# Performance work log

Measured on AMD Instinct MI355X. Metric: run time of the kernel, lower is better.

The kernel has to match this reference:

```python
import jax, jax.numpy as jnp
import numpy as np

N = 100000      # nodes (single node type)
R = 4           # relations
E = 800000      # edges per relation (avg in-degree ~32)
D_IN, D_H, D_OUT = 256, 64, 16


def setup_inputs() -> dict:
    key = jax.random.key(0)
    ks = jax.random.split(key, 9)
    x = jax.random.normal(ks[0], (N, D_IN), dtype=jnp.float32)
    src = jax.random.randint(ks[1], (R, E), 0, N, dtype=jnp.int32)
    dst = jax.random.randint(ks[2], (R, E), 0, N, dtype=jnp.int32)
    s_in = 1.0 / np.sqrt(D_IN)
    s_h = 1.0 / np.sqrt(D_H)
    W1 = jax.random.normal(ks[3], (R, D_IN, D_H), dtype=jnp.float32) * s_in
    L1w = jax.random.normal(ks[4], (D_IN, D_H), dtype=jnp.float32) * s_in
    L1b = jnp.zeros((D_H,), dtype=jnp.float32)
    W2 = jax.random.normal(ks[5], (R, D_H, D_OUT), dtype=jnp.float32) * s_h
    L2w = jax.random.normal(ks[6], (D_H, D_OUT), dtype=jnp.float32) * s_h
    L2b = jnp.zeros((D_OUT,), dtype=jnp.float32)
    return {"x": x, "src": src, "dst": dst, "W1": W1, "L1w": L1w,
            "L1b": L1b, "W2": W2, "L2w": L2w, "L2b": L2b}


def _rel_graph_conv(h, src, dst, W):
    """Per-relation GEMM + gather + scatter-add + right-normalize, summed over relations.
    h: [N, d_in]; src/dst: [R, E]; W: [R, d_in, d_out] -> [N, d_out]
    """
    hw = jnp.einsum('nd,rdh->rnh', h, W)  # transform first (d_out small), then gather

    def agg(hr, s, d):
        deg = jax.ops.segment_sum(jnp.ones((E,), hr.dtype), d, num_segments=N)
        msg = jax.ops.segment_sum(hr[s], d, num_segments=N)  # [N, d_out]
        return msg / jnp.maximum(deg, 1.0)[:, None]          # norm='right'

    return jnp.sum(jax.vmap(agg)(hw, src, dst), axis=0)


def reference(x, src, dst, W1, L1w, L1b, W2, L2w, L2b):
    # Layer 1: relation conv + self-loop linear + ReLU (dropout = eval/identity)
    h = _rel_graph_conv(x, src, dst, W1) + x @ L1w + L1b
    h = jax.nn.relu(h)
    # Layer 2: no activation
    out = _rel_graph_conv(h, src, dst, W2) + h @ L2w + L2b
    return out
```

## Files before the change

### kernel.cpp

```cpp
#include <hip/hip_runtime.h>


constexpr int NN = 100000, RR = 4, EE = 800000;
constexpr int RE = RR * EE;
constexpr int NBKT = (NN + 63) / 64;
constexpr int BCAP = 3072;
constexpr int NG1 = (NN + 63) / 64;
constexpr int CHUNK = 8192;
constexpr int NB = (RE + CHUNK - 1) / CHUNK;
constexpr int EPT = CHUNK / 512;

typedef short bf16x8 __attribute__((ext_vector_type(8)));
typedef float f32x4 __attribute__((ext_vector_type(4)));

__device__ inline unsigned short f2bf(float f) {
  unsigned u = __float_as_uint(f);
  u += 0x7FFF + ((u >> 16) & 1);
  return (unsigned short)(u >> 16);
}
__device__ inline float bf2f(unsigned short s) {
  return __uint_as_float(((unsigned)s) << 16);
}

__global__ __launch_bounds__(256) void prep_w_kernel(const float* __restrict__ W1,
                                                     const float* __restrict__ L1w,
                                                     const float* __restrict__ W2,
                                                     const float* __restrict__ L2w,
                                                     unsigned short* __restrict__ BT1,
                                                     unsigned short* __restrict__ BT2) {
  int idx = blockIdx.x * 256 + threadIdx.x;
  if (idx < 320 * 256) {
    int n = idx >> 8, k = idx & 255;
    float v = (n < 256) ? W1[((size_t)((n >> 6) * 256 + k)) * 64 + (n & 63)]
                        : L1w[(size_t)k * 64 + (n - 256)];
    BT1[idx] = f2bf(v);
  } else {
    int j = idx - 320 * 256;
    if (j < 80 * 64) {
      int n = j >> 6, k = j & 63;
      float v = (n < 64) ? W2[((size_t)((n >> 4) * 64 + k)) * 16 + (n & 15)]
                         : L2w[(size_t)k * 16 + (n - 64)];
      BT2[j] = f2bf(v);
    }
  }
}

__global__ __launch_bounds__(512) void fused1_kernel(const float* __restrict__ x,
                                                     const unsigned short* __restrict__ BT1,
                                                     const float* __restrict__ L1b,
                                                     const int* __restrict__ src,
                                                     const int* __restrict__ dst,
                                                     int* __restrict__ gcur,
                                                     int* __restrict__ binned,
                                                     unsigned short* __restrict__ hwcat,
                                                     unsigned short* __restrict__ h) {
  __shared__ char lds[49152];
  const int bid = blockIdx.x;
  const int t = threadIdx.x;
  const bool is_bin = (bid % 5 == 0) && (bid / 5 < NB);

  if (is_bin) {
    int* hist = (int*)lds;
    int* base = hist + NBKT;
    for (int k = t; k < NBKT; k += 512) hist[k] = 0;
    __syncthreads();
    const int e0 = (bid / 5) * CHUNK + t;
    int dl[EPT], sl[EPT];
#pragma unroll
    for (int i = 0; i < EPT; ++i) {
      int fl = e0 + i * 512;
      dl[i] = -1;
      if (fl < RE) {
        dl[i] = dst[fl];
        sl[i] = src[fl];
        atomicAdd(&hist[dl[i] >> 6], 1);
      }
    }
    __syncthreads();
    for (int k = t; k < NBKT; k += 512) {
      int hv = hist[k];
      base[k] = hv ? atomicAdd(&gcur[k], hv) : 0;
      hist[k] = 0;
    }
    __syncthreads();
#pragma unroll
    for (int i = 0; i < EPT; ++i) {
      if (dl[i] < 0) continue;
      int fl = e0 + i * 512;
      int r = fl / EE;
      int b = dl[i] >> 6;
      int off = atomicAdd(&hist[b], 1);
      int p = base[b] + off;
      if (p < BCAP) binned[(size_t)b * BCAP + p] = (sl[i] << 2) | r | ((dl[i] & 63) << 19);
    }
    return;
  }

  int nbins = (bid + 4) / 5;
  if (nbins > NB) nbins = NB;
  const int m0 = (bid - nbins) * 64;
  char* Al = lds;
  char* Bl = lds + 64 * 64 * 2;
  const int wid = t >> 6, lane = t & 63;
  const int wm = wid >> 2, wn = wid & 3;
  const int l15 = lane & 15, g = lane >> 4;

  f32x4 acc[2][5];
#pragma unroll
  for (int i = 0; i < 2; ++i)
#pragma unroll
    for (int j = 0; j < 5; ++j) acc[i][j] = (f32x4){0.f, 0.f, 0.f, 0.f};

  for (int kc = 0; kc < 4; ++kc) {
    if (kc) __syncthreads();
#pragma unroll
    for (int it = 0; it < 2; ++it) {
      int fl = t + 512 * it;
      int row = fl >> 4, kq = (fl & 15) * 4;
      int rg = m0 + row;
      float4 v = (rg < NN) ? *(const float4*)(x + (size_t)rg * 256 + kc * 64 + kq)
                           : make_float4(0.f, 0.f, 0.f, 0.f);
      ushort4 pck = {f2bf(v.x), f2bf(v.y), f2bf(v.z), f2bf(v.w)};
      int wb = ((row * 64 + kq) * 2) ^ ((row & 7) << 4);
      *(ushort4*)(Al + wb) = pck;
    }
#pragma unroll
    for (int it = 0; it < 5; ++it) {
      int fl = t + 512 * it;
      int n = fl >> 3, i8 = (fl & 7) * 8;
      uint4 u = *(const uint4*)(BT1 + (size_t)n * 256 + kc * 64 + i8);
      int wb = ((n * 64 + i8) * 2) ^ ((n & 7) << 4);
      *(uint4*)(Bl + wb) = u;
    }
    __syncthreads();
#pragma unroll
    for (int ks = 0; ks < 2; ++ks) {
      bf16x8 af[2], bfr[5];
#pragma unroll
      for (int mi = 0; mi < 2; ++mi) {
        int row = wm * 32 + mi * 16 + l15;
        int byte = ((row * 64 + ks * 32 + g * 8) * 2) ^ ((row & 7) << 4);
        af[mi] = *(const bf16x8*)(Al + byte);
      }
#pragma unroll
      for (int ni = 0; ni < 5; ++ni) {
        int n = wn * 80 + ni * 16 + l15;
        int byte = ((n * 64 + ks * 32 + g * 8) * 2) ^ ((n & 7) << 4);
        bfr[ni] = *(const bf16x8*)(Bl + byte);
      }
#pragma unroll
      for (int mi = 0; mi < 2; ++mi)
#pragma unroll
        for (int ni = 0; ni < 5; ++ni)
          acc[mi][ni] = __builtin_amdgcn_mfma_f32_16x16x32_bf16(af[mi], bfr[ni], acc[mi][ni], 0, 0, 0);
    }
  }
#pragma unroll
  for (int mi = 0; mi < 2; ++mi) {
    int rbase = m0 + wm * 32 + mi * 16 + 4 * g;
#pragma unroll
    for (int ni = 0; ni < 5; ++ni) {
      int n0 = wn * 80 + ni * 16;
      int n = n0 + l15;
#pragma unroll
      for (int e = 0; e < 4; ++e) {
        int row = rbase + e;
        if (row >= NN) continue;
        float v = acc[mi][ni][e];
        if (n0 < 256) hwcat[(size_t)row * 256 + n] = f2bf(v);
        else h[(size_t)row * 64 + (n - 256)] = f2bf(v + L1b[n - 256]);
      }
    }
  }
}

__global__ __launch_bounds__(256) void pull1_kernel(const unsigned short* __restrict__ h,
                                                    const unsigned short* __restrict__ hwcat,
                                                    const int* __restrict__ binned,
                                                    const int* __restrict__ gcur,
                                                    const unsigned short* __restrict__ BT2,
                                                    const float* __restrict__ L2b,
                                                    unsigned short* __restrict__ hw2,
                                                    float* __restrict__ out) {
  __shared__ int csr[BCAP];
  __shared__ int cnt[256];
  __shared__ int off[256];
  __shared__ float winv[256];
  __shared__ int tot[64];
  __shared__ char Al[64 * 64 * 2];
  const int t = threadIdx.x, bkt = blockIdx.x;
  const int wid = t >> 6, lane = t & 63;
  const int l15 = lane & 15, g = lane >> 4;

  int count = gcur[bkt];
  if (count > BCAP) count = BCAP;
  const int* edges = binned + (size_t)bkt * BCAP;

  cnt[t] = 0;
  __syncthreads();
  for (int i = t; i < count; i += 256) {
    int w = edges[i];
    atomicAdd(&cnt[((w >> 19) & 63) * 4 + (w & 3)], 1);
  }
  __syncthreads();
  off[t] = cnt[t];
  __syncthreads();
  for (int s = 1; s < 256; s <<= 1) {
    int v = (t >= s) ? off[t - s] : 0;
    __syncthreads();
    off[t] += v;
    __syncthreads();
  }
  int excl = off[t] - cnt[t];
  winv[t] = 1.0f / (float)(cnt[t] > 1 ? cnt[t] : 1);
  __syncthreads();
  off[t] = excl;
  cnt[t] = excl;
  __syncthreads();
  if (t < 64) tot[t] = ((t == 63) ? count : off[(t + 1) * 4]) - off[t * 4];
  __syncthreads();
  for (int i = t; i < count; i += 256) {
    int w = edges[i];
    int k = ((w >> 19) & 63) * 4 + (w & 3);
    int p = atomicAdd(&cnt[k], 1);
    csr[p] = w & 0x7FFFF;
  }
  __syncthreads();

  const int slot = lane >> 3, cpart = lane & 7;
  for (int ii = 0; ii < 16; ++ii) {
    int nloc = wid * 16 + ii;
    int beg = off[nloc * 4];
    int total = tot[nloc];
    float acc[8] = {0.f, 0.f, 0.f, 0.f, 0.f, 0.f, 0.f, 0.f};
    for (int p0 = 0; p0 < total; p0 += 8) {
      int j = p0 + slot;
      bool pr = j < total;
      int key = pr ? csr[beg + j] : 0;
      float wv = pr ? winv[nloc * 4 + (key & 3)] : 0.f;
      uint4 u = *(const uint4*)(hwcat + (size_t)key * 64 + cpart * 8);
#pragma unroll
      for (int q = 0; q < 4; ++q) {
        unsigned uu = (&u.x)[q];
        acc[q * 2]     = fmaf(wv, bf2f((unsigned short)(uu & 0xffffu)), acc[q * 2]);
        acc[q * 2 + 1] = fmaf(wv, bf2f((unsigned short)(uu >> 16)), acc[q * 2 + 1]);
      }
    }
#pragma unroll
    for (int m = 8; m <= 32; m <<= 1)
#pragma unroll
      for (int q = 0; q < 8; ++q) acc[q] += __shfl_xor(acc[q], m);
    if (slot == 0) {
      int gn = bkt * 64 + nloc;
      unsigned pk[4];
      uint4 hu = make_uint4(0, 0, 0, 0);
      if (gn < NN) hu = *(const uint4*)(h + (size_t)gn * 64 + cpart * 8);
#pragma unroll
      for (int q = 0; q < 4; ++q) {
        unsigned a = (&hu.x)[q];
        float v0 = acc[q * 2]     + bf2f((unsigned short)(a & 0xffffu));
        float v1 = acc[q * 2 + 1] + bf2f((unsigned short)(a >> 16));
        pk[q] = (unsigned)f2bf(fmaxf(v0, 0.f)) | ((unsigned)f2bf(fmaxf(v1, 0.f)) << 16);
      }
      int wb = ((nloc * 64 + cpart * 8) * 2) ^ ((nloc & 7) << 4);
      *(uint4*)(Al + wb) = make_uint4(pk[0], pk[1], pk[2], pk[3]);
    }
  }
  __syncthreads();

  char* Bl = (char*)csr;
#pragma unroll
  for (int it = 0; it < 3; ++it) {
    int fl = t + 256 * it;
    if (fl < 640) {
      int n = fl >> 3, i8 = (fl & 7) * 8;
      uint4 u = *(const uint4*)(BT2 + (size_t)n * 64 + i8);
      int wb = ((n * 64 + i8) * 2) ^ ((n & 7) << 4);
      *(uint4*)(Bl + wb) = u;
    }
  }
  __syncthreads();

  f32x4 acc2[5];
#pragma unroll
  for (int j = 0; j < 5; ++j) acc2[j] = (f32x4){0.f, 0.f, 0.f, 0.f};
#pragma unroll
  for (int ks = 0; ks < 2; ++ks) {
    int ra = wid * 16 + l15;
    int byte = ((ra * 64 + ks * 32 + g * 8) * 2) ^ ((ra & 7) << 4);
    bf16x8 af = *(const bf16x8*)(Al + byte);
#pragma unroll
    for (int ni = 0; ni < 5; ++ni) {
      int n = ni * 16 + l15;
      int nb = ((n * 64 + ks * 32 + g * 8) * 2) ^ ((n & 7) << 4);
      bf16x8 bfr = *(const bf16x8*)(Bl + nb);
      acc2[ni] = __builtin_amdgcn_mfma_f32_16x16x32_bf16(af, bfr, acc2[ni], 0, 0, 0);
    }
  }
  int rb = wid * 16 + 4 * g;
#pragma unroll
  for (int ni = 0; ni < 5; ++ni) {
    int n0 = ni * 16;
    int n = n0 + l15;
#pragma unroll
    for (int e = 0; e < 4; ++e) {
      int gno = bkt * 64 + rb + e;
      if (gno >= NN) continue;
      float vv = acc2[ni][e];
      if (n0 < 64) hw2[(size_t)gno * 64 + n] = f2bf(vv);
      else out[(size_t)gno * 16 + (n - 64)] = vv + L2b[n - 64];
    }
  }
}

__global__ __launch_bounds__(256) void pull2_kernel(const unsigned short* __restrict__ hw2,
                                                    const int* __restrict__ binned,
                                                    const int* __restrict__ gcur,
                                                    float* __restrict__ out) {
  __shared__ int csr[BCAP];
  __shared__ int cnt[256];
  __shared__ int off[256];
  __shared__ float winv[256];
  __shared__ int tot[64];
  __shared__ float ot[64][16];
  const int t = threadIdx.x, bkt = blockIdx.x;
  const int wid = t >> 6, lane = t & 63;

  int count = gcur[bkt];
  if (count > BCAP) count = BCAP;
  const int* edges = binned + (size_t)bkt * BCAP;

  cnt[t] = 0;
  __syncthreads();
  for (int i = t; i < count; i += 256) {
    int w = edges[i];
    atomicAdd(&cnt[((w >> 19) & 63) * 4 + (w & 3)], 1);
  }
  __syncthreads();
  off[t] = cnt[t];
  __syncthreads();
  for (int s = 1; s < 256; s <<= 1) {
    int v = (t >= s) ? off[t - s] : 0;
    __syncthreads();
    off[t] += v;
    __syncthreads();
  }
  int excl = off[t] - cnt[t];
  winv[t] = 1.0f / (float)(cnt[t] > 1 ? cnt[t] : 1);
  __syncthreads();
  off[t] = excl;
  cnt[t] = excl;
  __syncthreads();
  if (t < 64) tot[t] = ((t == 63) ? count : off[(t + 1) * 4]) - off[t * 4];
  __syncthreads();
  for (int i = t; i < count; i += 256) {
    int w = edges[i];
    int k = ((w >> 19) & 63) * 4 + (w & 3);
    int p = atomicAdd(&cnt[k], 1);
    csr[p] = w & 0x7FFFF;
  }
  __syncthreads();

  const int slot = lane >> 2, cpart = lane & 3;
  for (int ii = 0; ii < 16; ++ii) {
    int nloc = wid * 16 + ii;
    int beg = off[nloc * 4];
    int total = tot[nloc];
    float acc[4] = {0.f, 0.f, 0.f, 0.f};
    for (int p0 = 0; p0 < total; p0 += 16) {
      int j = p0 + slot;
      bool pr = j < total;
      int key = pr ? csr[beg + j] : 0;
      float wv = pr ? winv[nloc * 4 + (key & 3)] : 0.f;
      uint2 u = *(const uint2*)(hw2 + (size_t)key * 16 + cpart * 4);
      acc[0] = fmaf(wv, bf2f((unsigned short)(u.x & 0xffffu)), acc[0]);
      acc[1] = fmaf(wv, bf2f((unsigned short)(u.x >> 16)), acc[1]);
      acc[2] = fmaf(wv, bf2f((unsigned short)(u.y & 0xffffu)), acc[2]);
      acc[3] = fmaf(wv, bf2f((unsigned short)(u.y >> 16)), acc[3]);
    }
#pragma unroll
    for (int m = 4; m <= 32; m <<= 1)
#pragma unroll
      for (int q = 0; q < 4; ++q) acc[q] += __shfl_xor(acc[q], m);
    if (slot == 0)
      *(float4*)&ot[nloc][cpart * 4] = make_float4(acc[0], acc[1], acc[2], acc[3]);
  }
  __syncthreads();

  int row = t >> 2, q = t & 3;
  int gn = bkt * 64 + row;
  if (gn < NN) {
    float4 o = *(float4*)(out + (size_t)gn * 16 + q * 4);
    float4 a = *(float4*)&ot[row][q * 4];
    o.x += a.x; o.y += a.y; o.z += a.z; o.w += a.w;
    *(float4*)(out + (size_t)gn * 16 + q * 4) = o;
  }
}

extern "C" void kernel_launch(void* const* d_in, const int* in_sizes, int n_in,
                              void* d_out, int out_size, void* d_ws, size_t ws_size,
                              hipStream_t stream) {
  const float* x   = (const float*)d_in[0];
  const int*   src = (const int*)d_in[1];
  const int*   dst = (const int*)d_in[2];
  const float* W1  = (const float*)d_in[3];
  const float* L1w = (const float*)d_in[4];
  const float* L1b = (const float*)d_in[5];
  const float* W2  = (const float*)d_in[6];
  const float* L2w = (const float*)d_in[7];
  const float* L2b = (const float*)d_in[8];
  float* out = (float*)d_out;

  char* p = (char*)d_ws;
  int* binned = (int*)p;                      p += (size_t)NBKT * BCAP * 4;
  int* gcur   = (int*)p;                      p += 8192;
  unsigned short* hwcat = (unsigned short*)p; p += (size_t)NN * 256 * 2;
  unsigned short* h = (unsigned short*)p;     p += (size_t)NN * 64 * 2;
  unsigned short* hw2 = (unsigned short*)p;   p += (size_t)NN * 64 * 2;
  unsigned short* BT1 = (unsigned short*)p;   p += 320 * 256 * 2;
  unsigned short* BT2 = (unsigned short*)p;   p += 80 * 64 * 2;
  if ((size_t)(p - (char*)d_ws) > ws_size) return;

  hipMemsetAsync(gcur, 0, NBKT * 4, stream);
  prep_w_kernel<<<(320 * 256 + 80 * 64 + 255) / 256, 256, 0, stream>>>(W1, L1w, W2, L2w, BT1, BT2);
  fused1_kernel<<<NG1 + NB, 512, 0, stream>>>(x, BT1, L1b, src, dst, gcur, binned, hwcat, h);
  pull1_kernel<<<NBKT, 256, 0, stream>>>(h, hwcat, binned, gcur, BT2, L2b, hw2, out);
  pull2_kernel<<<NBKT, 256, 0, stream>>>(hw2, binned, gcur, out);
}
```

Measured before the change: 229.7 us.

## Sort binned edges locally in LDS before coalesced global scatter

The binning blocks now prefix-scan the per-bucket histogram, sort each chunk's edges by bucket in LDS, and then write them to the global bins in bucket-contiguous order, so the global stores are more coalesced than the earlier random scatter. The chunk size is halved and the interleave ratio of binning to GEMM blocks changes from 1:4 to 1:2 so the LDS staging fits. This adds a block scan and extra LDS traffic and launches more binning blocks, each with more global atomics per edge than before.

```diff
diff --git a/kernel.cpp b/kernel.cpp
--- a/kernel.cpp
+++ b/kernel.cpp
@@ -6,7 +6,7 @@
 constexpr int NBKT = (NN + 63) / 64;
 constexpr int BCAP = 3072;
 constexpr int NG1 = (NN + 63) / 64;
-constexpr int CHUNK = 8192;
+constexpr int CHUNK = 4096;
 constexpr int NB = (RE + CHUNK - 1) / CHUNK;
 constexpr int EPT = CHUNK / 512;
 
@@ -57,14 +57,20 @@
   __shared__ char lds[49152];
   const int bid = blockIdx.x;
   const int t = threadIdx.x;
-  const bool is_bin = (bid % 5 == 0) && (bid / 5 < NB);
+  const bool is_bin = (bid % 3 == 0) && (bid / 3 < NB);
 
   if (is_bin) {
-    int* hist = (int*)lds;
-    int* base = hist + NBKT;
+    int* hist   = (int*)lds;
+    int* delta  = (int*)(lds + 6400);
+    int* sorted = (int*)(lds + 12800);
+    short* bkt16 = (short*)(lds + 29184);
+    int* wsum   = (int*)(lds + 37376);
+    int* ptots  = (int*)(lds + 37440);
+    const int wid = t >> 6, lane = t & 63;
+
     for (int k = t; k < NBKT; k += 512) hist[k] = 0;
     __syncthreads();
-    const int e0 = (bid / 5) * CHUNK + t;
+    const int e0 = (bid / 3) * CHUNK + t;
     int dl[EPT], sl[EPT];
 #pragma unroll
     for (int i = 0; i < EPT; ++i) {
@@ -77,10 +83,40 @@
       }
     }
     __syncthreads();
-    for (int k = t; k < NBKT; k += 512) {
-      int hv = hist[k];
-      base[k] = hv ? atomicAdd(&gcur[k], hv) : 0;
-      hist[k] = 0;
+    int cnt4[4];
+    int s = 0;
+#pragma unroll
+    for (int j = 0; j < 4; ++j) {
+      int b = t * 4 + j;
+      cnt4[j] = (b < NBKT) ? hist[b] : 0;
+      s += cnt4[j];
+    }
+    int xs = s;
+#pragma unroll
+    for (int d = 1; d < 64; d <<= 1) {
+      int y = __shfl_up(xs, d);
+      if (lane >= d) xs += y;
+    }
+    if (lane == 63) wsum[wid] = xs;
+    __syncthreads();
+    int add = 0;
+#pragma unroll
+    for (int w = 0; w < 8; ++w)
+      if (w < wid) add += wsum[w];
+    if (t == 511) *ptots = xs + add;
+    int lb = xs + add - s;
+#pragma unroll
+    for (int j = 0; j < 4; ++j) {
+      int b = t * 4 + j;
+      if (b < NBKT) {
+        int c = cnt4[j];
+        if (c > 0) {
+          int gb = atomicAdd(&gcur[b], c);
+          delta[b] = gb - lb;
+          hist[b] = lb;
+        }
+        lb += c;
+      }
     }
     __syncthreads();
 #pragma unroll
@@ -89,18 +125,28 @@
       int fl = e0 + i * 512;
       int r = fl / EE;
       int b = dl[i] >> 6;
-      int off = atomicAdd(&hist[b], 1);
-      int p = base[b] + off;
-      if (p < BCAP) binned[(size_t)b * BCAP + p] = (sl[i] << 2) | r | ((dl[i] & 63) << 19);
+      int p = atomicAdd(&hist[b], 1);
+      sorted[p] = (sl[i] << 2) | r | ((dl[i] & 63) << 19);
+      bkt16[p] = (short)b;
+    }
+    __syncthreads();
+    int ptot = *ptots;
+#pragma unroll
+    for (int i = 0; i < EPT; ++i) {
+      int p = t + i * 512;
+      if (p >= ptot) break;
+      int b = bkt16[p];
+      int inb = delta[b] + p;
+      if (inb < BCAP) binned[(size_t)b * BCAP + inb] = sorted[p];
     }
     return;
   }
 
-  int nbins = (bid + 4) / 5;
+  int nbins = (bid + 2) / 3;
   if (nbins > NB) nbins = NB;
   const int m0 = (bid - nbins) * 64;
   char* Al = lds;
-  char* Bl = lds + 64 * 64 * 2;
+  char* Bl = lds + 8192;
   const int wid = t >> 6, lane = t & 63;
   const int wm = wid >> 2, wn = wid & 3;
   const int l15 = lane & 15, g = lane >> 4;
```

New measurement: 241.1 us. +5.0%, slower.

## Replace single-pass edge binning with two-pass coarse-then-fine radix scatter

Applied to the files above, without the earlier changes.

Edge binning now runs as two radix passes. The fused kernel sorts each chunk locally by 49 coarse buckets (2048 destinations each) and writes contiguous runs into a coarse buffer. A new pass2 kernel then splits each coarse bucket into 32 fine 64-node bins. The aim is to replace the scattered per-edge global writes and the 1563-entry histogram with coalesced block-sorted writes and fewer global atomics. In exchange it adds an extra kernel launch and a full read/write of the edge list through the coarse buffer.

```diff
diff --git a/kernel.cpp b/kernel.cpp
--- a/kernel.cpp
+++ b/kernel.cpp
@@ -5,8 +5,11 @@
 constexpr int RE = RR * EE;
 constexpr int NBKT = (NN + 63) / 64;
 constexpr int BCAP = 3072;
+constexpr int NCOARSE = 49;
+constexpr int CCAP = 69632;
+constexpr int NCH = 17;
 constexpr int NG1 = (NN + 63) / 64;
-constexpr int CHUNK = 8192;
+constexpr int CHUNK = 4096;
 constexpr int NB = (RE + CHUNK - 1) / CHUNK;
 constexpr int EPT = CHUNK / 512;
 
@@ -50,21 +53,26 @@
                                                      const float* __restrict__ L1b,
                                                      const int* __restrict__ src,
                                                      const int* __restrict__ dst,
-                                                     int* __restrict__ gcur,
-                                                     int* __restrict__ binned,
+                                                     int* __restrict__ gcoarse,
+                                                     int* __restrict__ cbuf,
                                                      unsigned short* __restrict__ hwcat,
                                                      unsigned short* __restrict__ h) {
   __shared__ char lds[49152];
   const int bid = blockIdx.x;
   const int t = threadIdx.x;
-  const bool is_bin = (bid % 5 == 0) && (bid / 5 < NB);
+  const bool is_bin = (bid % 3 == 0) && (bid / 3 < NB);
 
   if (is_bin) {
     int* hist = (int*)lds;
-    int* base = hist + NBKT;
-    for (int k = t; k < NBKT; k += 512) hist[k] = 0;
-    __syncthreads();
-    const int e0 = (bid / 5) * CHUNK + t;
+    int* cur = hist + 64;
+    int* delta = cur + 64;
+    int* sorted = delta + 64;
+    unsigned char* cb = (unsigned char*)(sorted + 4096);
+    const int fid = bid / 3;
+
+    if (t < 64) hist[t] = 0;
+    __syncthreads();
+    const int e0 = fid * CHUNK + t;
     int dl[EPT], sl[EPT];
 #pragma unroll
     for (int i = 0; i < EPT; ++i) {
@@ -73,14 +81,24 @@
       if (fl < RE) {
         dl[i] = dst[fl];
         sl[i] = src[fl];
-        atomicAdd(&hist[dl[i] >> 6], 1);
-      }
-    }
-    __syncthreads();
-    for (int k = t; k < NBKT; k += 512) {
-      int hv = hist[k];
-      base[k] = hv ? atomicAdd(&gcur[k], hv) : 0;
-      hist[k] = 0;
+        atomicAdd(&hist[dl[i] >> 11], 1);
+      }
+    }
+    __syncthreads();
+    if (t < 64) {
+      int c = (t < NCOARSE) ? hist[t] : 0;
+      int xs = c;
+#pragma unroll
+      for (int d = 1; d < 64; d <<= 1) {
+        int y = __shfl_up(xs, d);
+        if (t >= d) xs += y;
+      }
+      int excl = xs - c;
+      if (t < NCOARSE) {
+        cur[t] = excl;
+        int gb = (c > 0) ? atomicAdd(&gcoarse[t], c) : 0;
+        delta[t] = gb - excl;
+      }
     }
     __syncthreads();
 #pragma unroll
@@ -88,19 +106,31 @@
       if (dl[i] < 0) continue;
       int fl = e0 + i * 512;
       int r = fl / EE;
-      int b = dl[i] >> 6;
-      int off = atomicAdd(&hist[b], 1);
-      int p = base[b] + off;
-      if (p < BCAP) binned[(size_t)b * BCAP + p] = (sl[i] << 2) | r | ((dl[i] & 63) << 19);
+      int cg = dl[i] >> 11;
+      int p = atomicAdd(&cur[cg], 1);
+      sorted[p] = (sl[i] << 2) | r | ((dl[i] & 2047) << 19);
+      cb[p] = (unsigned char)cg;
+    }
+    __syncthreads();
+    int ptot = RE - fid * CHUNK;
+    if (ptot > CHUNK) ptot = CHUNK;
+#pragma unroll
+    for (int i = 0; i < EPT; ++i) {
+      int p = t + i * 512;
+      if (p < ptot) {
+        int cg = cb[p];
+        int inb = delta[cg] + p;
+        if (inb < CCAP) cbuf[(size_t)cg * CCAP + inb] = sorted[p];
+      }
     }
     return;
   }
 
-  int nbins = (bid + 4) / 5;
+  int nbins = (bid + 2) / 3;
   if (nbins > NB) nbins = NB;
   const int m0 = (bid - nbins) * 64;
   char* Al = lds;
-  char* Bl = lds + 64 * 64 * 2;
+  char* Bl = lds + 8192;
   const int wid = t >> 6, lane = t & 63;
   const int wm = wid >> 2, wn = wid & 3;
   const int l15 = lane & 15, g = lane >> 4;
@@ -170,6 +200,71 @@
         if (n0 < 256) hwcat[(size_t)row * 256 + n] = f2bf(v);
         else h[(size_t)row * 64 + (n - 256)] = f2bf(v + L1b[n - 256]);
       }
+    }
+  }
+}
+
+__global__ __launch_bounds__(512) void pass2_kernel(const int* __restrict__ cbuf,
+                                                    const int* __restrict__ gcoarse,
+                                                    int* __restrict__ gcur,
+                                                    int* __restrict__ binned) {
+  __shared__ int hist32[32], cur32[32], delta32[32];
+  __shared__ int sorted[4096];
+  __shared__ unsigned char cb[4096];
+  const int t = threadIdx.x;
+  const int g = blockIdx.x / NCH, ch = blockIdx.x % NCH;
+  int count = gcoarse[g];
+  if (count > CCAP) count = CCAP;
+  const int base = ch * 4096;
+  int nhere = count - base;
+  if (nhere <= 0) return;
+  if (nhere > 4096) nhere = 4096;
+
+  if (t < 32) hist32[t] = 0;
+  __syncthreads();
+  int wl[8], fl8[8];
+#pragma unroll
+  for (int i = 0; i < 8; ++i) {
+    int j = t + i * 512;
+    fl8[i] = -1;
+    if (j < nhere) {
+      int w = cbuf[(size_t)g * CCAP + base + j];
+      wl[i] = w;
+      fl8[i] = (w >> 25) & 31;
+      atomicAdd(&hist32[fl8[i]], 1);
+    }
+  }
+  __syncthreads();
+  if (t < 32) {
+    int c = hist32[t];
+    int xs = c;
+#pragma unroll
+    for (int d = 1; d < 32; d <<= 1) {
+      int y = __shfl_up(xs, d);
+      if (t >= d) xs += y;
+    }
+    int excl = xs - c;
+    cur32[t] = excl;
+    int gb = (c > 0) ? atomicAdd(&gcur[g * 32 + t], c) : 0;
+    delta32[t] = gb - excl;
+  }
+  __syncthreads();
+#pragma unroll
+  for (int i = 0; i < 8; ++i) {
+    if (fl8[i] < 0) continue;
+    int p = atomicAdd(&cur32[fl8[i]], 1);
+    int w = wl[i];
+    sorted[p] = (w & 0x7FFFF) | (((w >> 19) & 63) << 19);
+    cb[p] = (unsigned char)fl8[i];
+  }
+  __syncthreads();
+#pragma unroll
+  for (int i = 0; i < 8; ++i) {
+    int p = t + i * 512;
+    if (p < nhere) {
+      int f = cb[p];
+      int inb = delta32[f] + p;
+      if (inb < BCAP) binned[(size_t)(g * 32 + f) * BCAP + inb] = sorted[p];
     }
   }
 }
@@ -413,7 +508,9 @@
 
   char* p = (char*)d_ws;
   int* binned = (int*)p;                      p += (size_t)NBKT * BCAP * 4;
-  int* gcur   = (int*)p;                      p += 8192;
+  int* gcur   = (int*)p;                      p += 49 * 32 * 4;
+  int* gcoarse = (int*)p;                     p += 64 * 4;
+  int* cbuf   = (int*)p;                      p += (size_t)NCOARSE * CCAP * 4;
   unsigned short* hwcat = (unsigned short*)p; p += (size_t)NN * 256 * 2;
   unsigned short* h = (unsigned short*)p;     p += (size_t)NN * 64 * 2;
   unsigned short* hw2 = (unsigned short*)p;   p += (size_t)NN * 64 * 2;
@@ -421,9 +518,10 @@
   unsigned short* BT2 = (unsigned short*)p;   p += 80 * 64 * 2;
   if ((size_t)(p - (char*)d_ws) > ws_size) return;
 
-  hipMemsetAsync(gcur, 0, NBKT * 4, stream);
+  hipMemsetAsync(gcur, 0, (49 * 32 + 64) * 4, stream);
   prep_w_kernel<<<(320 * 256 + 80 * 64 + 255) / 256, 256, 0, stream>>>(W1, L1w, W2, L2w, BT1, BT2);
-  fused1_kernel<<<NG1 + NB, 512, 0, stream>>>(x, BT1, L1b, src, dst, gcur, binned, hwcat, h);
+  fused1_kernel<<<NG1 + NB, 512, 0, stream>>>(x, BT1, L1b, src, dst, gcoarse, cbuf, hwcat, h);
+  pass2_kernel<<<NCOARSE * NCH, 512, 0, stream>>>(cbuf, gcoarse, gcur, binned);
   pull1_kernel<<<NBKT, 256, 0, stream>>>(h, hwcat, binned, gcur, BT2, L2b, hw2, out);
   pull2_kernel<<<NBKT, 256, 0, stream>>>(hw2, binned, gcur, out);
 }
```

After: 233.4 us. No clear change (+1.6%).
